# Optimization experiments

Measured on AMD Instinct MI355X. Metric: run time of the kernel, lower is better.

The kernel has to match this reference:

```python
import jax, jax.numpy as jnp
import numpy as np

N_FFT = 1024
HOP = 512


def _overlap_add_50pct(frames):
    """Stateful 50% overlap-add. frames: (B, N, n_fft) -> (B, N, hop).
    Each frame is split into (curr, next); output[t] = curr[t] + next[t-1]."""
    xs = jnp.moveaxis(frames, 1, 0)  # (N, B, n_fft) for scan over frames

    def step(carry, x):
        x_curr = x[..., :HOP]
        x_next = x[..., HOP:]
        return x_next, x_curr + carry

    init = jnp.zeros((xs.shape[1], HOP), dtype=frames.dtype)
    _, ys = jax.lax.scan(step, init, xs)  # ys: (N, B, hop)
    return jnp.moveaxis(ys, 0, 1)  # (B, N, hop)


def _istft(re, im):
    spec = jax.lax.complex(re, im)               # (B, N, n_fft//2+1)
    frames = jnp.fft.irfft(spec, n=N_FFT, axis=-1)  # (B, N, n_fft), real IFFT
    frames = frames * jnp.asarray(0.5, frames.dtype)  # MulHalf (window_fn=None path)
    return _overlap_add_50pct(frames)            # (B, N, hop)


def setup_inputs() -> dict:
    key = jax.random.key(0)
    k1, k2 = jax.random.split(key)
    B, N = 8, 4000
    re = jax.random.normal(k1, (B, N, N_FFT // 2 + 1), dtype=jnp.float32)
    im = jax.random.normal(k2, (B, N, N_FFT // 2 + 1), dtype=jnp.float32)
    return {"re": re, "im": im}


def reference(re, im):
    return _istft(re, im)
```

## Files before the change

### kernel.cpp

```cpp
#include <hip/hip_runtime.h>
#include <math.h>

#define NBINS 513
#define NROWS 4000
#define BATCH 8
#define FPB   15
#define NITER 4

__device__ __forceinline__ void cmul(float& ar, float& ai, float br, float bi) {
    const float tr = ar * br - ai * bi;
    ai = ar * bi + ai * br;
    ar = tr;
}

__device__ __forceinline__ void idft8(float* xr, float* xi) {
    const float S = 0.70710678118654752440f;
    float er[4], ei[4], orr[4], oi[4];
    #pragma unroll
    for (int j = 0; j < 4; ++j) {
        er[j]  = xr[j] + xr[j+4];  ei[j] = xi[j] + xi[j+4];
        orr[j] = xr[j] - xr[j+4];  oi[j] = xi[j] - xi[j+4];
    }
    const float f1r = S * (orr[1] - oi[1]), f1i = S * (orr[1] + oi[1]);
    const float f2r = -oi[2],               f2i = orr[2];
    const float f3r = S * (-orr[3] - oi[3]), f3i = S * (orr[3] - oi[3]);
    {
        const float eer = er[0]+er[2], eei = ei[0]+ei[2];
        const float eor = er[0]-er[2], eoi = ei[0]-ei[2];
        const float oer = er[1]+er[3], oei = ei[1]+ei[3];
        const float oor = er[1]-er[3], ooi = ei[1]-ei[3];
        xr[0] = eer + oer;  xi[0] = eei + oei;
        xr[2] = eor - ooi;  xi[2] = eoi + oor;
        xr[4] = eer - oer;  xi[4] = eei - oei;
        xr[6] = eor + ooi;  xi[6] = eoi - oor;
    }
    {
        const float eer = orr[0]+f2r, eei = oi[0]+f2i;
        const float eor = orr[0]-f2r, eoi = oi[0]-f2i;
        const float oer = f1r+f3r,    oei = f1i+f3i;
        const float oor = f1r-f3r,    ooi = f1i-f3i;
        xr[1] = eer + oer;  xi[1] = eei + oei;
        xr[3] = eor - ooi;  xi[3] = eoi + oor;
        xr[5] = eer - oer;  xi[5] = eei - oei;
        xr[7] = eor + ooi;  xi[7] = eoi - oor;
    }
}

__global__ __launch_bounds__(256) void istft_kernel(
    const float* __restrict__ re, const float* __restrict__ im,
    float* __restrict__ out)
{
    __shared__ float2 tw2[512];
    __shared__ float2 ex2[4][512];

    const int tid = threadIdx.x;
    const int u   = tid & 63;
    const int g   = tid >> 6;
    const int b   = blockIdx.y;
    const int t0  = blockIdx.x * FPB;

    {
        const float w0 = 6.283185307179586476925f / 1024.0f;
        float s, c;
        int k = tid;
        sincosf(w0 * (float)k, &s, &c); tw2[k] = make_float2(c, s);
        k += 256;
        sincosf(w0 * (float)k, &s, &c); tw2[k] = make_float2(c, s);
    }
    __syncthreads();

    const int k1 = u >> 3;
    const int k2 = u & 7;

    float2 cc[4];
    #pragma unroll
    for (int m = 0; m < 4; ++m) cc[m] = make_float2(0.f, 0.f);

    for (int it = 0; it < NITER; ++it) {
        const int t = t0 - 1 + it * 4 + g;

        float zr8[8], zi8[8];
        if (t >= 0 && t < NROWS) {
            const size_t base = ((size_t)b * NROWS + (size_t)t) * NBINS;
            const float* rp = re + base;
            const float* ip = im + base;
            const float F = 4.8828125e-4f;
            #pragma unroll
            for (int j = 0; j < 8; ++j) {
                const int k = u + 64 * j;
                float xr = rp[k], xi = ip[k];
                float rc, ic;
                if (k == 0) { xi = 0.f; rc = rp[512]; ic = 0.f; }
                else        { rc = rp[512 - k]; ic = -ip[512 - k]; }
                const float er = F * (xr + rc), ei = F * (xi + ic);
                const float hr = F * (xr - rc), hi = F * (xi - ic);
                const float2 w = tw2[k];
                const float o_r = w.x * hr - w.y * hi;
                const float o_i = w.x * hi + w.y * hr;
                zr8[j] = er - o_i;
                zi8[j] = ei + o_r;
            }
        } else {
            #pragma unroll
            for (int j = 0; j < 8; ++j) { zr8[j] = 0.f; zi8[j] = 0.f; }
        }

        idft8(zr8, zi8);
        {
            const float2 w1 = tw2[16 * k1];
            float tr = w1.x, ti = w1.y;
            #pragma unroll
            for (int m0 = 1; m0 < 8; ++m0) {
                cmul(zr8[m0], zi8[m0], tr, ti);
                cmul(tr, ti, w1.x, w1.y);
            }
        }
        #pragma unroll
        for (int m0 = 0; m0 < 8; ++m0) {
            const int a = 64 * m0 + 8 * ((k1 ^ m0) & 7) + k2;
            ex2[g][a] = make_float2(zr8[m0], zi8[m0]);
        }
        __syncthreads();
        #pragma unroll
        for (int kk = 0; kk < 8; ++kk) {
            const int a = 64 * k1 + 8 * ((kk ^ k1) & 7) + k2;
            const float2 v = ex2[g][a];
            zr8[kk] = v.x; zi8[kk] = v.y;
        }
        idft8(zr8, zi8);
        {
            const float2 b0 = tw2[2 * k2 * k1];
            const float2 ws = tw2[16 * k2];
            float tr = b0.x, ti = b0.y;
            #pragma unroll
            for (int m1 = 0; m1 < 8; ++m1) {
                cmul(zr8[m1], zi8[m1], tr, ti);
                cmul(tr, ti, ws.x, ws.y);
            }
        }
        __syncthreads();
        #pragma unroll
        for (int m1 = 0; m1 < 8; ++m1) {
            const int a = 64 * k2 + 8 * ((m1 ^ k2) & 7) + k1;
            ex2[g][a] = make_float2(zr8[m1], zi8[m1]);
        }
        __syncthreads();
        #pragma unroll
        for (int kk = 0; kk < 8; ++kk) {
            const int a = 64 * kk + 8 * ((k1 ^ kk) & 7) + k2;
            const float2 v = ex2[g][a];
            zr8[kk] = v.x; zi8[kk] = v.y;
        }
        idft8(zr8, zi8);
        __syncthreads();

        #pragma unroll
        for (int m = 0; m < 4; ++m)
            ex2[g][u + 64 * m] = make_float2(zr8[m + 4], zi8[m + 4]);
        __syncthreads();

        const bool emit = (t >= t0) && (t < NROWS);
        if (emit) {
            float2* orow = (float2*)(out + ((size_t)b * NROWS + (size_t)t) * 512);
            #pragma unroll
            for (int m = 0; m < 4; ++m) {
                float2 pv = (g == 0) ? cc[m] : ex2[g - 1][u + 64 * m];
                orow[u + 64 * m] = make_float2(zr8[m] + pv.x, zi8[m] + pv.y);
            }
        }
        if (g == 0) {
            #pragma unroll
            for (int m = 0; m < 4; ++m) cc[m] = ex2[3][u + 64 * m];
        }
        __syncthreads();
    }
}

extern "C" void kernel_launch(void* const* d_in, const int* in_sizes, int n_in,
                              void* d_out, int out_size, void* d_ws, size_t ws_size,
                              hipStream_t stream) {
    const float* re = (const float*)d_in[0];
    const float* im = (const float*)d_in[1];
    float* out = (float*)d_out;
    dim3 grid((NROWS + FPB - 1) / FPB, BATCH);
    istft_kernel<<<grid, 256, 0, stream>>>(re, im, out);
}
```

Before: 51.41 us.

## Give each wavefront its own chain of frames to drop block barriers

Each 64-thread wavefront now processes a run of 8 consecutive frames on its own and carries the overlap-add tail in registers. The shared-memory transposes are private to the wavefront, so every block-wide __syncthreads is removed. The shared twiddle table is replaced by per-thread sincosf values held in registers. In exchange, one extra frame per 8 outputs is recomputed instead of one per 15, the grid has fewer blocks, and each wave works through its frames in sequence, which may reduce memory-level parallelism.

```diff
diff --git a/kernel.cpp b/kernel.cpp
--- a/kernel.cpp
+++ b/kernel.cpp
@@ -4,13 +4,14 @@
 #define NBINS 513
 #define NROWS 4000
 #define BATCH 8
-#define FPB   15
-#define NITER 4
+#define FPW   8
+#define CPB   4
+#define CHAINS_PER_BATCH (NROWS / FPW)
 
 __device__ __forceinline__ void cmul(float& ar, float& ai, float br, float bi) {
-    const float tr = ar * br - ai * bi;
+    const float t = ar * br - ai * bi;
     ai = ar * bi + ai * br;
-    ar = tr;
+    ar = t;
 }
 
 __device__ __forceinline__ void idft8(float* xr, float* xi) {
@@ -50,37 +51,40 @@
     const float* __restrict__ re, const float* __restrict__ im,
     float* __restrict__ out)
 {
-    __shared__ float2 tw2[512];
-    __shared__ float2 ex2[4][512];
+    __shared__ float2 ex2[CPB][512];
 
     const int tid = threadIdx.x;
     const int u   = tid & 63;
     const int g   = tid >> 6;
     const int b   = blockIdx.y;
-    const int t0  = blockIdx.x * FPB;
-
-    {
-        const float w0 = 6.283185307179586476925f / 1024.0f;
-        float s, c;
-        int k = tid;
-        sincosf(w0 * (float)k, &s, &c); tw2[k] = make_float2(c, s);
-        k += 256;
-        sincosf(w0 * (float)k, &s, &c); tw2[k] = make_float2(c, s);
-    }
-    __syncthreads();
+    const int chain = blockIdx.x * CPB + g;
+    const int t0  = chain * FPW;
 
     const int k1 = u >> 3;
     const int k2 = u & 7;
+
+    const float w0 = 6.283185307179586476925f / 1024.0f;
+    float2 twp[8];
+    #pragma unroll
+    for (int j = 0; j < 8; ++j) {
+        float s, c; sincosf(w0 * (float)(u + 64 * j), &s, &c);
+        twp[j] = make_float2(c, s);
+    }
+    float2 wA, wB0, wBs;
+    {
+        float s, c;
+        sincosf(w0 * (float)(16 * k1), &s, &c);     wA  = make_float2(c, s);
+        sincosf(w0 * (float)(2 * k2 * k1), &s, &c); wB0 = make_float2(c, s);
+        sincosf(w0 * (float)(16 * k2), &s, &c);     wBs = make_float2(c, s);
+    }
 
     float2 cc[4];
     #pragma unroll
     for (int m = 0; m < 4; ++m) cc[m] = make_float2(0.f, 0.f);
 
-    for (int it = 0; it < NITER; ++it) {
-        const int t = t0 - 1 + it * 4 + g;
-
+    for (int t = t0 - 1; t < t0 + FPW; ++t) {
         float zr8[8], zi8[8];
-        if (t >= 0 && t < NROWS) {
+        if (t >= 0) {
             const size_t base = ((size_t)b * NROWS + (size_t)t) * NBINS;
             const float* rp = re + base;
             const float* ip = im + base;
@@ -94,9 +98,8 @@
                 else        { rc = rp[512 - k]; ic = -ip[512 - k]; }
                 const float er = F * (xr + rc), ei = F * (xi + ic);
                 const float hr = F * (xr - rc), hi = F * (xi - ic);
-                const float2 w = tw2[k];
-                const float o_r = w.x * hr - w.y * hi;
-                const float o_i = w.x * hi + w.y * hr;
+                const float o_r = twp[j].x * hr - twp[j].y * hi;
+                const float o_i = twp[j].x * hi + twp[j].y * hr;
                 zr8[j] = er - o_i;
                 zi8[j] = ei + o_r;
             }
@@ -107,72 +110,50 @@
 
         idft8(zr8, zi8);
         {
-            const float2 w1 = tw2[16 * k1];
-            float tr = w1.x, ti = w1.y;
+            float tr = wA.x, ti = wA.y;
             #pragma unroll
             for (int m0 = 1; m0 < 8; ++m0) {
                 cmul(zr8[m0], zi8[m0], tr, ti);
-                cmul(tr, ti, w1.x, w1.y);
+                cmul(tr, ti, wA.x, wA.y);
             }
         }
         #pragma unroll
-        for (int m0 = 0; m0 < 8; ++m0) {
-            const int a = 64 * m0 + 8 * ((k1 ^ m0) & 7) + k2;
-            ex2[g][a] = make_float2(zr8[m0], zi8[m0]);
-        }
-        __syncthreads();
+        for (int m0 = 0; m0 < 8; ++m0)
+            ex2[g][64 * m0 + 8 * ((k1 ^ m0) & 7) + k2] = make_float2(zr8[m0], zi8[m0]);
         #pragma unroll
         for (int kk = 0; kk < 8; ++kk) {
-            const int a = 64 * k1 + 8 * ((kk ^ k1) & 7) + k2;
-            const float2 v = ex2[g][a];
+            const float2 v = ex2[g][64 * k1 + 8 * ((kk ^ k1) & 7) + k2];
             zr8[kk] = v.x; zi8[kk] = v.y;
         }
+
         idft8(zr8, zi8);
         {
-            const float2 b0 = tw2[2 * k2 * k1];
-            const float2 ws = tw2[16 * k2];
-            float tr = b0.x, ti = b0.y;
+            float tr = wB0.x, ti = wB0.y;
             #pragma unroll
             for (int m1 = 0; m1 < 8; ++m1) {
                 cmul(zr8[m1], zi8[m1], tr, ti);
-                cmul(tr, ti, ws.x, ws.y);
+                cmul(tr, ti, wBs.x, wBs.y);
             }
         }
-        __syncthreads();
         #pragma unroll
-        for (int m1 = 0; m1 < 8; ++m1) {
-            const int a = 64 * k2 + 8 * ((m1 ^ k2) & 7) + k1;
-            ex2[g][a] = make_float2(zr8[m1], zi8[m1]);
-        }
-        __syncthreads();
+        for (int m1 = 0; m1 < 8; ++m1)
+            ex2[g][64 * k2 + 8 * ((m1 ^ k2) & 7) + k1] = make_float2(zr8[m1], zi8[m1]);
         #pragma unroll
         for (int kk = 0; kk < 8; ++kk) {
-            const int a = 64 * kk + 8 * ((k1 ^ kk) & 7) + k2;
-            const float2 v = ex2[g][a];
+            const float2 v = ex2[g][64 * kk + 8 * ((k1 ^ kk) & 7) + k2];
             zr8[kk] = v.x; zi8[kk] = v.y;
         }
+
         idft8(zr8, zi8);
-        __syncthreads();
 
-        #pragma unroll
-        for (int m = 0; m < 4; ++m)
-            ex2[g][u + 64 * m] = make_float2(zr8[m + 4], zi8[m + 4]);
-        __syncthreads();
-
-        const bool emit = (t >= t0) && (t < NROWS);
-        if (emit) {
+        if (t >= t0) {
             float2* orow = (float2*)(out + ((size_t)b * NROWS + (size_t)t) * 512);
             #pragma unroll
-            for (int m = 0; m < 4; ++m) {
-                float2 pv = (g == 0) ? cc[m] : ex2[g - 1][u + 64 * m];
-                orow[u + 64 * m] = make_float2(zr8[m] + pv.x, zi8[m] + pv.y);
-            }
+            for (int m = 0; m < 4; ++m)
+                orow[u + 64 * m] = make_float2(zr8[m] + cc[m].x, zi8[m] + cc[m].y);
         }
-        if (g == 0) {
-            #pragma unroll
-            for (int m = 0; m < 4; ++m) cc[m] = ex2[3][u + 64 * m];
-        }
-        __syncthreads();
+        #pragma unroll
+        for (int m = 0; m < 4; ++m) cc[m] = make_float2(zr8[m + 4], zi8[m + 4]);
     }
 }
 
@@ -182,6 +163,6 @@
     const float* re = (const float*)d_in[0];
     const float* im = (const float*)d_in[1];
     float* out = (float*)d_out;
-    dim3 grid((NROWS + FPB - 1) / FPB, BATCH);
+    dim3 grid(CHAINS_PER_BATCH / CPB, BATCH);
     istft_kernel<<<grid, 256, 0, stream>>>(re, im, out);
 }
```

After: 48.98 us. 1.05x faster.
